# Kernel optimization log

Measured on AMD Instinct MI355X. Metric: run time of the kernel, lower is better.

The kernel has to match this reference:

```python
import jax, jax.numpy as jnp
import numpy as np
from jax import lax

EMBED_DIM = 128
N_RELATIONS = 64
N_ENTITIES = 100000
N_EDGES = 600000


def setup_inputs() -> dict:
    key = jax.random.key(0)
    k1, k2, k3, k4, k5, k6 = jax.random.split(key, 6)
    entity_emb = jax.random.normal(k1, (N_ENTITIES, EMBED_DIM), dtype=jnp.float32)
    heads = jax.random.randint(k2, (N_EDGES,), 0, N_ENTITIES)
    rels = jax.random.randint(k3, (N_EDGES,), 0, N_RELATIONS)
    tails = jax.random.randint(k4, (N_EDGES,), 0, N_ENTITIES)
    # learned params: relation embedding table (std=0.01) and square Linear weight (xavier)
    rel_embed_weight = 0.01 * jax.random.normal(k5, (N_RELATIONS, EMBED_DIM), dtype=jnp.float32)
    xavier = float(np.sqrt(6.0 / (EMBED_DIM + EMBED_DIM)))
    W = jax.random.uniform(k6, (EMBED_DIM, EMBED_DIM), dtype=jnp.float32, minval=-xavier, maxval=xavier)
    return {"entity_emb": entity_emb, "rel_embed_weight": rel_embed_weight, "W": W,
            "heads": heads, "rels": rels, "tails": tails}


def reference(entity_emb, rel_embed_weight, W, heads, rels, tails):
    n_entities = entity_emb.shape[0]
    # gather edge endpoint / relation embeddings: [E, D]
    e_h = entity_emb[heads]
    e_t = entity_emb[tails]
    e_r = rel_embed_weight[rels]
    # tanh-gated dot-product score per edge: [E]
    score = jnp.sum(e_t * jnp.tanh(e_h + e_r), axis=-1)
    # global max-shift (detached in torch) then per-head segment softmax
    score_exp = jnp.exp(score - lax.stop_gradient(jnp.max(score)))
    score_sum = jax.ops.segment_sum(score_exp, heads, num_segments=n_entities)
    attn = score_exp / (score_sum[heads] + 1e-10)
    # scatter-add attention-weighted messages back to head nodes: [N, D]
    agg = jax.ops.segment_sum(attn[:, None] * e_t, heads, num_segments=n_entities)
    # final Linear (no bias) + LeakyReLU(0.2); dropout is identity in eval mode
    out = (entity_emb + agg) @ W.T
    return jax.nn.leaky_relu(out, negative_slope=0.2)
```

## Files before the change

kernel.cpp:

```cpp
#include <hip/hip_runtime.h>
#include <math.h>

#define EMBED 128
#define BMAX 8192
#define LDSPAD 136

typedef __attribute__((ext_vector_type(8))) short short8;
typedef __attribute__((ext_vector_type(4))) short short4v;
typedef __attribute__((ext_vector_type(4))) float floatx4;

__device__ __forceinline__ float fast_tanh2(float x) {
    float e = __expf(2.0f * x);
    return 1.0f - 2.0f * __builtin_amdgcn_rcpf(1.0f + e);
}

__device__ __forceinline__ unsigned short f2b(float f) {
    union { float f; unsigned int u; } v; v.f = f;
    unsigned int r = v.u + 0x7FFFu + ((v.u >> 16) & 1u);
    return (unsigned short)(r >> 16);
}

__device__ __forceinline__ float b2f(short u) {
    union { float f; unsigned int i; } v;
    v.i = ((unsigned int)(unsigned short)u) << 16;
    return v.f;
}

__global__ __launch_bounds__(256) void k_cast_hist(
    const float* __restrict__ ent, const float* __restrict__ rel,
    short* __restrict__ entb, short* __restrict__ relb,
    const int* __restrict__ heads, int* __restrict__ cnt,
    int ngE, int ngR, int E)
{
    int stride = gridDim.x * 256;
    for (int g = blockIdx.x * 256 + threadIdx.x; g < ngE + ngR; g += stride) {
        const float4* src; short* dst;
        if (g < ngE) { src = (const float4*)ent + (size_t)g * 2; dst = entb + (size_t)g * 8; }
        else { int g2 = g - ngE; src = (const float4*)rel + (size_t)g2 * 2; dst = relb + (size_t)g2 * 8; }
        float4 a = src[0], b = src[1];
        short8 o;
        o[0] = (short)f2b(a.x); o[1] = (short)f2b(a.y); o[2] = (short)f2b(a.z); o[3] = (short)f2b(a.w);
        o[4] = (short)f2b(b.x); o[5] = (short)f2b(b.y); o[6] = (short)f2b(b.z); o[7] = (short)f2b(b.w);
        *(short8*)dst = o;
    }
    for (int e = blockIdx.x * 256 + threadIdx.x; e < E; e += stride)
        atomicAdd(cnt + heads[e], 1);
}

__global__ __launch_bounds__(1024) void k_scan1(
    const int* __restrict__ cnt, int* __restrict__ offs,
    int* __restrict__ bsum, int N)
{
    __shared__ int buf[1024];
    int i = blockIdx.x * 1024 + threadIdx.x;
    int v = (i < N) ? cnt[i] : 0;
    buf[threadIdx.x] = v;
    __syncthreads();
    for (int off = 1; off < 1024; off <<= 1) {
        int x = (threadIdx.x >= (unsigned)off) ? buf[threadIdx.x - off] : 0;
        __syncthreads();
        buf[threadIdx.x] += x;
        __syncthreads();
    }
    if (i < N) offs[i] = buf[threadIdx.x] - v;
    if (threadIdx.x == 1023) bsum[blockIdx.x] = buf[1023];
}

__global__ __launch_bounds__(1024) void k_scan2(int* __restrict__ bsum, int nb)
{
    __shared__ int buf[1024];
    int v = (threadIdx.x < (unsigned)nb) ? bsum[threadIdx.x] : 0;
    buf[threadIdx.x] = v;
    __syncthreads();
    for (int off = 1; off < 1024; off <<= 1) {
        int x = (threadIdx.x >= (unsigned)off) ? buf[threadIdx.x - off] : 0;
        __syncthreads();
        buf[threadIdx.x] += x;
        __syncthreads();
    }
    if (threadIdx.x < (unsigned)nb) bsum[threadIdx.x] = buf[threadIdx.x] - v;
}

__global__ __launch_bounds__(256) void k_scan3(
    int* __restrict__ offs, const int* __restrict__ bsum,
    int* __restrict__ cursor, int N)
{
    int i = blockIdx.x * 256 + threadIdx.x;
    if (i < N) {
        int o = offs[i] + bsum[i >> 10];
        offs[i] = o;
        cursor[i] = o;
    }
}

__global__ __launch_bounds__(256) void k_csr(
    const int* __restrict__ heads, const int* __restrict__ rels,
    const int* __restrict__ tails, int* __restrict__ cursor,
    int2* __restrict__ tr, int E)
{
    int e = blockIdx.x * 256 + threadIdx.x;
    if (e >= E) return;
    int pos = atomicAdd(cursor + heads[e], 1);
    tr[pos] = make_int2(tails[e], rels[e]);
}

__global__ __launch_bounds__(256) void k_fused(
    const short* __restrict__ entb, const short* __restrict__ relb,
    const int* __restrict__ offs, const int* __restrict__ cnt,
    const int2* __restrict__ tr,
    short* __restrict__ accb, float* __restrict__ mh, float* __restrict__ lh,
    float* __restrict__ blockmax, int N, int R)
{
    __shared__ short rl[64 * EMBED];
    const int tid = threadIdx.x;
    if (R <= 64) {
        int nch = R * 16;
        for (int i = tid; i < nch; i += 256)
            ((short8*)rl)[i] = ((const short8*)relb)[i];
    }
    __syncthreads();
    const short* relsrc = (R <= 64) ? (const short*)rl : relb;

    const int lane = tid & 15;
    int head = blockIdx.x * 16 + (tid >> 4);
    float m = -INFINITY;
    if (head < N) {
        int start = offs[head];
        int c     = cnt[head];
        short8 hh = *((const short8*)(entb + (size_t)head * EMBED) + lane);
        float hf[8];
        #pragma unroll
        for (int i = 0; i < 8; ++i) hf[i] = b2f(hh[i]);
        float l = 0.f;
        float acc[8] = {0,0,0,0,0,0,0,0};
        for (int base = 0; base < c; base += 16) {
            int rem = c - base;
            int mm  = rem < 16 ? rem : 16;
            int2 trv = make_int2(0, 0);
            if (lane < mm) trv = tr[start + base + lane];
            for (int j = 0; j < mm; ++j) {
                int t = __shfl(trv.x, j, 16);
                int r = __shfl(trv.y, j, 16);
                short8 vt = *((const short8*)(entb + (size_t)t * EMBED) + lane);
                short8 vr = *((const short8*)(relsrc + (size_t)r * EMBED) + lane);
                float s = 0.f;
                #pragma unroll
                for (int i = 0; i < 8; ++i)
                    s += b2f(vt[i]) * fast_tanh2(hf[i] + b2f(vr[i]));
                s += __shfl_xor(s, 1, 16);
                s += __shfl_xor(s, 2, 16);
                s += __shfl_xor(s, 4, 16);
                s += __shfl_xor(s, 8, 16);
                float mn    = fmaxf(m, s);
                float alpha = __expf(m - mn);
                float p     = __expf(s - mn);
                l = l * alpha + p;
                #pragma unroll
                for (int q = 0; q < 8; ++q)
                    acc[q] = acc[q] * alpha + p * b2f(vt[q]);
                m = mn;
            }
        }
        short8 o;
        #pragma unroll
        for (int q = 0; q < 8; ++q) o[q] = (short)f2b(acc[q]);
        *((short8*)(accb + (size_t)head * EMBED) + lane) = o;
        if (lane == 0) { mh[head] = m; lh[head] = l; }
    }
    __shared__ float smax[256];
    smax[tid] = m;
    __syncthreads();
    for (int off = 128; off > 0; off >>= 1) {
        if (tid < off) smax[tid] = fmaxf(smax[tid], smax[tid + off]);
        __syncthreads();
    }
    if (tid == 0) blockmax[blockIdx.x] = smax[0];
}

__global__ __launch_bounds__(256) void k_maxred(
    const float* __restrict__ blockmax, float* __restrict__ Mout, int n)
{
    __shared__ float smax[256];
    float m = -INFINITY;
    for (int i = threadIdx.x; i < n; i += 256) m = fmaxf(m, blockmax[i]);
    smax[threadIdx.x] = m;
    __syncthreads();
    for (int off = 128; off > 0; off >>= 1) {
        if ((int)threadIdx.x < off)
            smax[threadIdx.x] = fmaxf(smax[threadIdx.x], smax[threadIdx.x + off]);
        __syncthreads();
    }
    if (threadIdx.x == 0) Mout[0] = smax[0];
}

__global__ __launch_bounds__(256) void k_gemm_f(
    const short* __restrict__ entb, const short* __restrict__ accb,
    const float* __restrict__ mh, const float* __restrict__ lh,
    const float* __restrict__ Mptr, const float* __restrict__ W,
    float* __restrict__ out, int N)
{
    __shared__ short xs[128 * LDSPAD];
    __shared__ short ws[128 * LDSPAD];
    const int tid = threadIdx.x;
    const int n0  = blockIdx.x * 128;
    const float M = Mptr[0];

    #pragma unroll
    for (int it = 0; it < 16; ++it) {
        int f4 = it * 256 + tid;
        int row = f4 >> 5, col4 = f4 & 31;
        float4 v = ((const float4*)W)[f4];
        short4v b; b[0] = (short)f2b(v.x); b[1] = (short)f2b(v.y);
                   b[2] = (short)f2b(v.z); b[3] = (short)f2b(v.w);
        *(short4v*)(ws + row * LDSPAD + col4 * 4) = b;
    }
    #pragma unroll
    for (int it = 0; it < 8; ++it) {
        int ch = it * 256 + tid;
        int row = ch >> 4, col8 = ch & 15;
        int g = n0 + row;
        short8 v = {0,0,0,0,0,0,0,0};
        if (g < N) {
            float inv = 1.0f / (lh[g] + 1e-10f * __expf(M - mh[g]));
            short8 e8 = *((const short8*)(entb + (size_t)g * EMBED) + col8);
            short8 a8 = *((const short8*)(accb + (size_t)g * EMBED) + col8);
            #pragma unroll
            for (int q = 0; q < 8; ++q)
                v[q] = (short)f2b(b2f(e8[q]) + b2f(a8[q]) * inv);
        }
        *(short8*)(xs + row * LDSPAD + col8 * 8) = v;
    }
    __syncthreads();

    const int wv   = tid >> 6;
    const int lane = tid & 63;
    const int n16  = lane & 15;
    const int quad = lane >> 4;

    floatx4 acc[2][8];
    #pragma unroll
    for (int rt = 0; rt < 2; ++rt)
        #pragma unroll
        for (int jt = 0; jt < 8; ++jt)
            acc[rt][jt] = (floatx4){0.f, 0.f, 0.f, 0.f};

    #pragma unroll
    for (int kc = 0; kc < 4; ++kc) {
        int koff = kc * 32 + quad * 8;
        short8 a0 = *(const short8*)(xs + (wv * 32      + n16) * LDSPAD + koff);
        short8 a1 = *(const short8*)(xs + (wv * 32 + 16 + n16) * LDSPAD + koff);
        #pragma unroll
        for (int jt = 0; jt < 8; ++jt) {
            short8 b = *(const short8*)(ws + (jt * 16 + n16) * LDSPAD + koff);
            acc[0][jt] = __builtin_amdgcn_mfma_f32_16x16x32_bf16(a0, b, acc[0][jt], 0, 0, 0);
            acc[1][jt] = __builtin_amdgcn_mfma_f32_16x16x32_bf16(a1, b, acc[1][jt], 0, 0, 0);
        }
    }

    #pragma unroll
    for (int rt = 0; rt < 2; ++rt) {
        int rowbase = n0 + wv * 32 + rt * 16 + quad * 4;
        #pragma unroll
        for (int r = 0; r < 4; ++r) {
            int grow = rowbase + r;
            if (grow < N) {
                float* o = out + (size_t)grow * EMBED + n16;
                #pragma unroll
                for (int jt = 0; jt < 8; ++jt) {
                    float v = acc[rt][jt][r];
                    o[jt * 16] = (v > 0.f) ? v : 0.2f * v;
                }
            }
        }
    }
}

extern "C" void kernel_launch(void* const* d_in, const int* in_sizes, int n_in,
                              void* d_out, int out_size, void* d_ws, size_t ws_size,
                              hipStream_t stream)
{
    const float* ent   = (const float*)d_in[0];
    const float* rel   = (const float*)d_in[1];
    const float* W     = (const float*)d_in[2];
    const int*   heads = (const int*)d_in[3];
    const int*   rels  = (const int*)d_in[4];
    const int*   tails = (const int*)d_in[5];
    const int E = in_sizes[3];
    const int N = in_sizes[0] / EMBED;
    const int R = in_sizes[1] / EMBED;
    float* out = (float*)d_out;

    short* accb     = (short*)d_ws;
    float* mh       = (float*)(accb + (size_t)N * EMBED);
    float* lh       = mh + N;
    int2*  tr       = (int2*)(lh + N);
    int*   cnt      = (int*)(tr + E);
    int*   offs     = cnt + N;
    int*   cursor   = offs + N;
    float* blockmax = (float*)(cursor + N);
    float* Mval     = blockmax + BMAX;
    int*   bsum     = (int*)(Mval + 1);
    short* entb     = (short*)(bsum + 1024);
    short* relb     = entb + (size_t)N * EMBED;

    const int nb  = (N + 1023) >> 10;
    const int ngh = (N + 15) / 16;

    hipMemsetAsync(cnt, 0, (size_t)N * sizeof(int), stream);

    int ngE = N * EMBED / 8, ngR = R * EMBED / 8;
    k_cast_hist<<<2048, 256, 0, stream>>>(ent, rel, entb, relb, heads, cnt, ngE, ngR, E);
    k_scan1<<<nb, 1024, 0, stream>>>(cnt, offs, bsum, N);
    k_scan2<<<1, 1024, 0, stream>>>(bsum, nb);
    k_scan3<<<(N + 255) / 256, 256, 0, stream>>>(offs, bsum, cursor, N);
    k_csr<<<(E + 255) / 256, 256, 0, stream>>>(heads, rels, tails, cursor, tr, E);
    k_fused<<<ngh, 256, 0, stream>>>(entb, relb, offs, cnt, tr, accb, mh, lh, blockmax, N, R);
    k_maxred<<<1, 256, 0, stream>>>(blockmax, Mval, ngh);
    k_gemm_f<<<(N + 127) / 128, 256, 0, stream>>>(entb, accb, mh, lh, Mval, W, out, N);
}
```

Baseline: 258.9 us.

## Use exp2-domain tanh/softmax, prefetch tails, warp scans, atomic global max

Relation embeddings are pre-scaled by 2*log2e and head features likewise, so tanh and the online softmax use exp2 directly with fewer multiplies. The next tail row is prefetched inside the edge loop to overlap gather latency. The LDS scans are replaced with wavefront shuffle scans, and the per-block max now goes through an ordered-int atomicMax, which removes the separate max-reduce kernel. W is cast to bf16 once in the cast kernel rather than in every GEMM block. Rounding the pre-scaled relation values to bf16 slightly changes numerics.

```diff
diff --git a/kernel.cpp b/kernel.cpp
--- a/kernel.cpp
+++ b/kernel.cpp
@@ -2,17 +2,14 @@
 #include <math.h>
 
 #define EMBED 128
-#define BMAX 8192
 #define LDSPAD 136
 
+#define TWO_LOG2E 2.8853900817779268f
+#define LOG2E     1.4426950408889634f
+
 typedef __attribute__((ext_vector_type(8))) short short8;
-typedef __attribute__((ext_vector_type(4))) short short4v;
 typedef __attribute__((ext_vector_type(4))) float floatx4;
-
-__device__ __forceinline__ float fast_tanh2(float x) {
-    float e = __expf(2.0f * x);
-    return 1.0f - 2.0f * __builtin_amdgcn_rcpf(1.0f + e);
-}
+typedef __attribute__((ext_vector_type(4))) unsigned int uint4v;
 
 __device__ __forceinline__ unsigned short f2b(float f) {
     union { float f; unsigned int u; } v; v.f = f;
@@ -27,20 +24,24 @@
 }
 
 __global__ __launch_bounds__(256) void k_cast_hist(
-    const float* __restrict__ ent, const float* __restrict__ rel,
-    short* __restrict__ entb, short* __restrict__ relb,
+    const float* __restrict__ ent, const float* __restrict__ rel, const float* __restrict__ W,
+    short* __restrict__ entb, short* __restrict__ relb, short* __restrict__ wb,
     const int* __restrict__ heads, int* __restrict__ cnt,
-    int ngE, int ngR, int E)
+    int ngE, int ngR, int ngW, int E)
 {
     int stride = gridDim.x * 256;
-    for (int g = blockIdx.x * 256 + threadIdx.x; g < ngE + ngR; g += stride) {
-        const float4* src; short* dst;
-        if (g < ngE) { src = (const float4*)ent + (size_t)g * 2; dst = entb + (size_t)g * 8; }
-        else { int g2 = g - ngE; src = (const float4*)rel + (size_t)g2 * 2; dst = relb + (size_t)g2 * 8; }
+    int total = ngE + ngR + ngW;
+    for (int g = blockIdx.x * 256 + threadIdx.x; g < total; g += stride) {
+        const float4* src; short* dst; float sc;
+        if (g < ngE)            { src = (const float4*)ent + (size_t)g * 2;              dst = entb + (size_t)g * 8;              sc = 1.0f; }
+        else if (g < ngE + ngR) { int g2 = g - ngE;       src = (const float4*)rel + (size_t)g2 * 2; dst = relb + (size_t)g2 * 8; sc = TWO_LOG2E; }
+        else                    { int g2 = g - ngE - ngR; src = (const float4*)W   + (size_t)g2 * 2; dst = wb   + (size_t)g2 * 8; sc = 1.0f; }
         float4 a = src[0], b = src[1];
         short8 o;
-        o[0] = (short)f2b(a.x); o[1] = (short)f2b(a.y); o[2] = (short)f2b(a.z); o[3] = (short)f2b(a.w);
-        o[4] = (short)f2b(b.x); o[5] = (short)f2b(b.y); o[6] = (short)f2b(b.z); o[7] = (short)f2b(b.w);
+        o[0] = (short)f2b(a.x * sc); o[1] = (short)f2b(a.y * sc);
+        o[2] = (short)f2b(a.z * sc); o[3] = (short)f2b(a.w * sc);
+        o[4] = (short)f2b(b.x * sc); o[5] = (short)f2b(b.y * sc);
+        o[6] = (short)f2b(b.z * sc); o[7] = (short)f2b(b.w * sc);
         *(short8*)dst = o;
     }
     for (int e = blockIdx.x * 256 + threadIdx.x; e < E; e += stride)
@@ -51,34 +52,60 @@
     const int* __restrict__ cnt, int* __restrict__ offs,
     int* __restrict__ bsum, int N)
 {
-    __shared__ int buf[1024];
-    int i = blockIdx.x * 1024 + threadIdx.x;
+    __shared__ int wsum[16];
+    const int tid = threadIdx.x;
+    int i = blockIdx.x * 1024 + tid;
     int v = (i < N) ? cnt[i] : 0;
-    buf[threadIdx.x] = v;
-    __syncthreads();
-    for (int off = 1; off < 1024; off <<= 1) {
-        int x = (threadIdx.x >= (unsigned)off) ? buf[threadIdx.x - off] : 0;
-        __syncthreads();
-        buf[threadIdx.x] += x;
-        __syncthreads();
-    }
-    if (i < N) offs[i] = buf[threadIdx.x] - v;
-    if (threadIdx.x == 1023) bsum[blockIdx.x] = buf[1023];
+    int x = v;
+    #pragma unroll
+    for (int d = 1; d < 64; d <<= 1) {
+        int y = __shfl_up(x, d, 64);
+        if ((tid & 63) >= d) x += y;
+    }
+    if ((tid & 63) == 63) wsum[tid >> 6] = x;
+    __syncthreads();
+    if (tid < 16) {
+        int w = wsum[tid];
+        #pragma unroll
+        for (int d = 1; d < 16; d <<= 1) {
+            int y = __shfl_up(w, d, 16);
+            if (tid >= d) w += y;
+        }
+        wsum[tid] = w;
+    }
+    __syncthreads();
+    int add = (tid >= 64) ? wsum[(tid >> 6) - 1] : 0;
+    int incl = x + add;
+    if (i < N) offs[i] = incl - v;
+    if (tid == 1023) bsum[blockIdx.x] = incl;
 }
 
 __global__ __launch_bounds__(1024) void k_scan2(int* __restrict__ bsum, int nb)
 {
-    __shared__ int buf[1024];
-    int v = (threadIdx.x < (unsigned)nb) ? bsum[threadIdx.x] : 0;
-    buf[threadIdx.x] = v;
-    __syncthreads();
-    for (int off = 1; off < 1024; off <<= 1) {
-        int x = (threadIdx.x >= (unsigned)off) ? buf[threadIdx.x - off] : 0;
-        __syncthreads();
-        buf[threadIdx.x] += x;
-        __syncthreads();
-    }
-    if (threadIdx.x < (unsigned)nb) bsum[threadIdx.x] = buf[threadIdx.x] - v;
+    __shared__ int wsum[16];
+    const int tid = threadIdx.x;
+    int v = (tid < nb) ? bsum[tid] : 0;
+    int x = v;
+    #pragma unroll
+    for (int d = 1; d < 64; d <<= 1) {
+        int y = __shfl_up(x, d, 64);
+        if ((tid & 63) >= d) x += y;
+    }
+    if ((tid & 63) == 63) wsum[tid >> 6] = x;
+    __syncthreads();
+    if (tid < 16) {
+        int w = wsum[tid];
+        #pragma unroll
+        for (int d = 1; d < 16; d <<= 1) {
+            int y = __shfl_up(w, d, 16);
+            if (tid >= d) w += y;
+        }
+        wsum[tid] = w;
+    }
+    __syncthreads();
+    int add = (tid >= 64) ? wsum[(tid >> 6) - 1] : 0;
+    int incl = x + add;
+    if (tid < nb) bsum[tid] = incl - v;
 }
 
 __global__ __launch_bounds__(256) void k_scan3(
@@ -109,7 +136,7 @@
     const int* __restrict__ offs, const int* __restrict__ cnt,
     const int2* __restrict__ tr,
     short* __restrict__ accb, float* __restrict__ mh, float* __restrict__ lh,
-    float* __restrict__ blockmax, int N, int R)
+    unsigned int* __restrict__ Mbits, int N, int R)
 {
     __shared__ short rl[64 * EMBED];
     const int tid = threadIdx.x;
@@ -127,10 +154,13 @@
     if (head < N) {
         int start = offs[head];
         int c     = cnt[head];
-        short8 hh = *((const short8*)(entb + (size_t)head * EMBED) + lane);
+        uint4v hu = *((const uint4v*)(entb + (size_t)head * EMBED) + lane);
         float hf[8];
         #pragma unroll
-        for (int i = 0; i < 8; ++i) hf[i] = b2f(hh[i]);
+        for (int p = 0; p < 4; ++p) {
+            hf[2*p]   = __uint_as_float(hu[p] << 16)          * TWO_LOG2E;
+            hf[2*p+1] = __uint_as_float(hu[p] & 0xFFFF0000u)  * TWO_LOG2E;
+        }
         float l = 0.f;
         float acc[8] = {0,0,0,0,0,0,0,0};
         for (int base = 0; base < c; base += 16) {
@@ -138,26 +168,46 @@
             int mm  = rem < 16 ? rem : 16;
             int2 trv = make_int2(0, 0);
             if (lane < mm) trv = tr[start + base + lane];
+            int t0 = __shfl(trv.x, 0, 16);
+            uint4v vtn = *((const uint4v*)(entb + (size_t)t0 * EMBED) + lane);
             for (int j = 0; j < mm; ++j) {
-                int t = __shfl(trv.x, j, 16);
+                uint4v vt = vtn;
+                if (j + 1 < mm) {
+                    int t2 = __shfl(trv.x, j + 1, 16);
+                    vtn = *((const uint4v*)(entb + (size_t)t2 * EMBED) + lane);
+                }
                 int r = __shfl(trv.y, j, 16);
-                short8 vt = *((const short8*)(entb + (size_t)t * EMBED) + lane);
-                short8 vr = *((const short8*)(relsrc + (size_t)r * EMBED) + lane);
-                float s = 0.f;
+                uint4v ru = *((const uint4v*)(relsrc + (size_t)r * EMBED) + lane);
+                float S = 0.f;
+                float vtf[8];
                 #pragma unroll
-                for (int i = 0; i < 8; ++i)
-                    s += b2f(vt[i]) * fast_tanh2(hf[i] + b2f(vr[i]));
-                s += __shfl_xor(s, 1, 16);
-                s += __shfl_xor(s, 2, 16);
-                s += __shfl_xor(s, 4, 16);
-                s += __shfl_xor(s, 8, 16);
-                float mn    = fmaxf(m, s);
-                float alpha = __expf(m - mn);
-                float p     = __expf(s - mn);
+                for (int p = 0; p < 4; ++p) {
+                    unsigned int tu = vt[p], rr = ru[p];
+                    float tlo = __uint_as_float(tu << 16);
+                    float thi = __uint_as_float(tu & 0xFFFF0000u);
+                    float xlo = hf[2*p]   + __uint_as_float(rr << 16);
+                    float xhi = hf[2*p+1] + __uint_as_float(rr & 0xFFFF0000u);
+                    float elo = exp2f(xlo);
+                    float ehi = exp2f(xhi);
+                    float clo = __builtin_amdgcn_rcpf(1.0f + elo);
+                    float chi = __builtin_amdgcn_rcpf(1.0f + ehi);
+                    S += tlo * (1.0f - 2.0f * clo);
+                    S += thi * (1.0f - 2.0f * chi);
+                    vtf[2*p]   = tlo;
+                    vtf[2*p+1] = thi;
+                }
+                S += __shfl_xor(S, 1, 16);
+                S += __shfl_xor(S, 2, 16);
+                S += __shfl_xor(S, 4, 16);
+                S += __shfl_xor(S, 8, 16);
+                float s2    = S * LOG2E;
+                float mn    = fmaxf(m, s2);
+                float alpha = exp2f(m - mn);
+                float p     = exp2f(s2 - mn);
                 l = l * alpha + p;
                 #pragma unroll
                 for (int q = 0; q < 8; ++q)
-                    acc[q] = acc[q] * alpha + p * b2f(vt[q]);
+                    acc[q] = acc[q] * alpha + p * vtf[q];
                 m = mn;
             }
         }
@@ -174,45 +224,32 @@
         if (tid < off) smax[tid] = fmaxf(smax[tid], smax[tid + off]);
         __syncthreads();
     }
-    if (tid == 0) blockmax[blockIdx.x] = smax[0];
-}
-
-__global__ __launch_bounds__(256) void k_maxred(
-    const float* __restrict__ blockmax, float* __restrict__ Mout, int n)
-{
-    __shared__ float smax[256];
-    float m = -INFINITY;
-    for (int i = threadIdx.x; i < n; i += 256) m = fmaxf(m, blockmax[i]);
-    smax[threadIdx.x] = m;
-    __syncthreads();
-    for (int off = 128; off > 0; off >>= 1) {
-        if ((int)threadIdx.x < off)
-            smax[threadIdx.x] = fmaxf(smax[threadIdx.x], smax[threadIdx.x + off]);
-        __syncthreads();
-    }
-    if (threadIdx.x == 0) Mout[0] = smax[0];
+    if (tid == 0) {
+        unsigned int u = __float_as_uint(smax[0]);
+        unsigned int key = (u & 0x80000000u) ? ~u : (u | 0x80000000u);
+        atomicMax(Mbits, key);
+    }
 }
 
 __global__ __launch_bounds__(256) void k_gemm_f(
     const short* __restrict__ entb, const short* __restrict__ accb,
     const float* __restrict__ mh, const float* __restrict__ lh,
-    const float* __restrict__ Mptr, const float* __restrict__ W,
+    const unsigned int* __restrict__ Mbits, const short* __restrict__ wb,
     float* __restrict__ out, int N)
 {
     __shared__ short xs[128 * LDSPAD];
     __shared__ short ws[128 * LDSPAD];
     const int tid = threadIdx.x;
     const int n0  = blockIdx.x * 128;
-    const float M = Mptr[0];
-
-    #pragma unroll
-    for (int it = 0; it < 16; ++it) {
-        int f4 = it * 256 + tid;
-        int row = f4 >> 5, col4 = f4 & 31;
-        float4 v = ((const float4*)W)[f4];
-        short4v b; b[0] = (short)f2b(v.x); b[1] = (short)f2b(v.y);
-                   b[2] = (short)f2b(v.z); b[3] = (short)f2b(v.w);
-        *(short4v*)(ws + row * LDSPAD + col4 * 4) = b;
+    unsigned int k = Mbits[0];
+    const float M2 = (k & 0x80000000u) ? __uint_as_float(k & 0x7FFFFFFFu)
+                                       : __uint_as_float(~k);
+
+    #pragma unroll
+    for (int it = 0; it < 8; ++it) {
+        int ch = it * 256 + tid;
+        int row = ch >> 4, col8 = ch & 15;
+        *(short8*)(ws + row * LDSPAD + col8 * 8) = ((const short8*)wb)[ch];
     }
     #pragma unroll
     for (int it = 0; it < 8; ++it) {
@@ -221,7 +258,7 @@
         int g = n0 + row;
         short8 v = {0,0,0,0,0,0,0,0};
         if (g < N) {
-            float inv = 1.0f / (lh[g] + 1e-10f * __expf(M - mh[g]));
+            float inv = 1.0f / (lh[g] + 1e-10f * exp2f(M2 - mh[g]));
             short8 e8 = *((const short8*)(entb + (size_t)g * EMBED) + col8);
             short8 a8 = *((const short8*)(accb + (size_t)g * EMBED) + col8);
             #pragma unroll
@@ -290,31 +327,31 @@
     const int R = in_sizes[1] / EMBED;
     float* out = (float*)d_out;
 
-    short* accb     = (short*)d_ws;
-    float* mh       = (float*)(accb + (size_t)N * EMBED);
-    float* lh       = mh + N;
-    int2*  tr       = (int2*)(lh + N);
-    int*   cnt      = (int*)(tr + E);
-    int*   offs     = cnt + N;
-    int*   cursor   = offs + N;
-    float* blockmax = (float*)(cursor + N);
-    float* Mval     = blockmax + BMAX;
-    int*   bsum     = (int*)(Mval + 1);
-    short* entb     = (short*)(bsum + 1024);
-    short* relb     = entb + (size_t)N * EMBED;
+    short* accb        = (short*)d_ws;
+    float* mh          = (float*)(accb + (size_t)N * EMBED);
+    float* lh          = mh + N;
+    int2*  tr          = (int2*)(lh + N);
+    int*   cnt         = (int*)(tr + E);
+    int*   offs        = cnt + N;
+    int*   cursor      = offs + N;
+    short* wb          = (short*)(cursor + N);
+    int*   bsum        = (int*)(wb + 16384);
+    unsigned int* Mbits = (unsigned int*)(bsum + 1024);
+    short* entb        = (short*)(Mbits + 4);
+    short* relb        = entb + (size_t)N * EMBED;
 
     const int nb  = (N + 1023) >> 10;
     const int ngh = (N + 15) / 16;
 
     hipMemsetAsync(cnt, 0, (size_t)N * sizeof(int), stream);
-
-    int ngE = N * EMBED / 8, ngR = R * EMBED / 8;
-    k_cast_hist<<<2048, 256, 0, stream>>>(ent, rel, entb, relb, heads, cnt, ngE, ngR, E);
+    hipMemsetAsync((void*)Mbits, 0, sizeof(unsigned int), stream);
+
+    int ngE = N * EMBED / 8, ngR = R * EMBED / 8, ngW = EMBED * EMBED / 8;
+    k_cast_hist<<<2048, 256, 0, stream>>>(ent, rel, W, entb, relb, wb, heads, cnt, ngE, ngR, ngW, E);
     k_scan1<<<nb, 1024, 0, stream>>>(cnt, offs, bsum, N);
     k_scan2<<<1, 1024, 0, stream>>>(bsum, nb);
     k_scan3<<<(N + 255) / 256, 256, 0, stream>>>(offs, bsum, cursor, N);
     k_csr<<<(E + 255) / 256, 256, 0, stream>>>(heads, rels, tails, cursor, tr, E);
-    k_fused<<<ngh, 256, 0, stream>>>(entb, relb, offs, cnt, tr, accb, mh, lh, blockmax, N, R);
-    k_maxred<<<1, 256, 0, stream>>>(blockmax, Mval, ngh);
-    k_gemm_f<<<(N + 127) / 128, 256, 0, stream>>>(entb, accb, mh, lh, Mval, W, out, N);
-}
+    k_fused<<<ngh, 256, 0, stream>>>(entb, relb, offs, cnt, tr, accb, mh, lh, Mbits, N, R);
+    k_gemm_f<<<(N + 127) / 128, 256, 0, stream>>>(entb, accb, mh, lh, Mbits, wb, out, N);
+}
```

New measurement: 281.5 us. +8.7%, slower.

## Precast W to bf16 once, use shuffle-based scans, and exp2 tanh

Applied to the files above, without the earlier changes.

Converts the weight matrix to bf16 once inside the cast kernel, so each GEMM block copies ready bf16 rows into LDS instead of loading fp32 and converting. Replaces the LDS Hillis-Steele scans with wavefront shuffle scans plus a small per-wave sum pass, which cuts the many block-wide barriers. Computes tanh through a direct exp2 builtin with a prescaled constant. The ideas are small and touch minor stages, so the overall gain may be limited. The workspace layout is shifted to make room for the bf16 weight buffer.

```diff
diff --git a/kernel.cpp b/kernel.cpp
--- a/kernel.cpp
+++ b/kernel.cpp
@@ -5,12 +5,15 @@
 #define BMAX 8192
 #define LDSPAD 136
 
+#define TWO_LOG2E 2.8853900817779268f
+
 typedef __attribute__((ext_vector_type(8))) short short8;
-typedef __attribute__((ext_vector_type(4))) short short4v;
 typedef __attribute__((ext_vector_type(4))) float floatx4;
 
+__device__ __forceinline__ float ex2(float x) { return __builtin_amdgcn_exp2f(x); }
+
 __device__ __forceinline__ float fast_tanh2(float x) {
-    float e = __expf(2.0f * x);
+    float e = ex2(TWO_LOG2E * x);
     return 1.0f - 2.0f * __builtin_amdgcn_rcpf(1.0f + e);
 }
 
@@ -27,16 +30,18 @@
 }
 
 __global__ __launch_bounds__(256) void k_cast_hist(
-    const float* __restrict__ ent, const float* __restrict__ rel,
-    short* __restrict__ entb, short* __restrict__ relb,
+    const float* __restrict__ ent, const float* __restrict__ rel, const float* __restrict__ W,
+    short* __restrict__ entb, short* __restrict__ relb, short* __restrict__ wb,
     const int* __restrict__ heads, int* __restrict__ cnt,
-    int ngE, int ngR, int E)
+    int ngE, int ngR, int ngW, int E)
 {
     int stride = gridDim.x * 256;
-    for (int g = blockIdx.x * 256 + threadIdx.x; g < ngE + ngR; g += stride) {
+    int total = ngE + ngR + ngW;
+    for (int g = blockIdx.x * 256 + threadIdx.x; g < total; g += stride) {
         const float4* src; short* dst;
-        if (g < ngE) { src = (const float4*)ent + (size_t)g * 2; dst = entb + (size_t)g * 8; }
-        else { int g2 = g - ngE; src = (const float4*)rel + (size_t)g2 * 2; dst = relb + (size_t)g2 * 8; }
+        if (g < ngE)            { src = (const float4*)ent + (size_t)g * 2;              dst = entb + (size_t)g * 8; }
+        else if (g < ngE + ngR) { int g2 = g - ngE;       src = (const float4*)rel + (size_t)g2 * 2; dst = relb + (size_t)g2 * 8; }
+        else                    { int g2 = g - ngE - ngR; src = (const float4*)W   + (size_t)g2 * 2; dst = wb   + (size_t)g2 * 8; }
         float4 a = src[0], b = src[1];
         short8 o;
         o[0] = (short)f2b(a.x); o[1] = (short)f2b(a.y); o[2] = (short)f2b(a.z); o[3] = (short)f2b(a.w);
@@ -51,34 +56,60 @@
     const int* __restrict__ cnt, int* __restrict__ offs,
     int* __restrict__ bsum, int N)
 {
-    __shared__ int buf[1024];
-    int i = blockIdx.x * 1024 + threadIdx.x;
+    __shared__ int wsum[16];
+    const int tid = threadIdx.x;
+    int i = blockIdx.x * 1024 + tid;
     int v = (i < N) ? cnt[i] : 0;
-    buf[threadIdx.x] = v;
-    __syncthreads();
-    for (int off = 1; off < 1024; off <<= 1) {
-        int x = (threadIdx.x >= (unsigned)off) ? buf[threadIdx.x - off] : 0;
-        __syncthreads();
-        buf[threadIdx.x] += x;
-        __syncthreads();
-    }
-    if (i < N) offs[i] = buf[threadIdx.x] - v;
-    if (threadIdx.x == 1023) bsum[blockIdx.x] = buf[1023];
+    int x = v;
+    #pragma unroll
+    for (int d = 1; d < 64; d <<= 1) {
+        int y = __shfl_up(x, d, 64);
+        if ((tid & 63) >= d) x += y;
+    }
+    if ((tid & 63) == 63) wsum[tid >> 6] = x;
+    __syncthreads();
+    if (tid < 16) {
+        int w = wsum[tid];
+        #pragma unroll
+        for (int d = 1; d < 16; d <<= 1) {
+            int y = __shfl_up(w, d, 16);
+            if (tid >= d) w += y;
+        }
+        wsum[tid] = w;
+    }
+    __syncthreads();
+    int add = (tid >= 64) ? wsum[(tid >> 6) - 1] : 0;
+    int incl = x + add;
+    if (i < N) offs[i] = incl - v;
+    if (tid == 1023) bsum[blockIdx.x] = incl;
 }
 
 __global__ __launch_bounds__(1024) void k_scan2(int* __restrict__ bsum, int nb)
 {
-    __shared__ int buf[1024];
-    int v = (threadIdx.x < (unsigned)nb) ? bsum[threadIdx.x] : 0;
-    buf[threadIdx.x] = v;
-    __syncthreads();
-    for (int off = 1; off < 1024; off <<= 1) {
-        int x = (threadIdx.x >= (unsigned)off) ? buf[threadIdx.x - off] : 0;
-        __syncthreads();
-        buf[threadIdx.x] += x;
-        __syncthreads();
-    }
-    if (threadIdx.x < (unsigned)nb) bsum[threadIdx.x] = buf[threadIdx.x] - v;
+    __shared__ int wsum[16];
+    const int tid = threadIdx.x;
+    int v = (tid < nb) ? bsum[tid] : 0;
+    int x = v;
+    #pragma unroll
+    for (int d = 1; d < 64; d <<= 1) {
+        int y = __shfl_up(x, d, 64);
+        if ((tid & 63) >= d) x += y;
+    }
+    if ((tid & 63) == 63) wsum[tid >> 6] = x;
+    __syncthreads();
+    if (tid < 16) {
+        int w = wsum[tid];
+        #pragma unroll
+        for (int d = 1; d < 16; d <<= 1) {
+            int y = __shfl_up(w, d, 16);
+            if (tid >= d) w += y;
+        }
+        wsum[tid] = w;
+    }
+    __syncthreads();
+    int add = (tid >= 64) ? wsum[(tid >> 6) - 1] : 0;
+    int incl = x + add;
+    if (tid < nb) bsum[tid] = incl - v;
 }
 
 __global__ __launch_bounds__(256) void k_scan3(
@@ -196,7 +227,7 @@
 __global__ __launch_bounds__(256) void k_gemm_f(
     const short* __restrict__ entb, const short* __restrict__ accb,
     const float* __restrict__ mh, const float* __restrict__ lh,
-    const float* __restrict__ Mptr, const float* __restrict__ W,
+    const float* __restrict__ Mptr, const short* __restrict__ wb,
     float* __restrict__ out, int N)
 {
     __shared__ short xs[128 * LDSPAD];
@@ -206,13 +237,10 @@
     const float M = Mptr[0];
 
     #pragma unroll
-    for (int it = 0; it < 16; ++it) {
-        int f4 = it * 256 + tid;
-        int row = f4 >> 5, col4 = f4 & 31;
-        float4 v = ((const float4*)W)[f4];
-        short4v b; b[0] = (short)f2b(v.x); b[1] = (short)f2b(v.y);
-                   b[2] = (short)f2b(v.z); b[3] = (short)f2b(v.w);
-        *(short4v*)(ws + row * LDSPAD + col4 * 4) = b;
+    for (int it = 0; it < 8; ++it) {
+        int ch = it * 256 + tid;
+        int row = ch >> 4, col8 = ch & 15;
+        *(short8*)(ws + row * LDSPAD + col8 * 8) = ((const short8*)wb)[ch];
     }
     #pragma unroll
     for (int it = 0; it < 8; ++it) {
@@ -299,8 +327,9 @@
     int*   cursor   = offs + N;
     float* blockmax = (float*)(cursor + N);
     float* Mval     = blockmax + BMAX;
-    int*   bsum     = (int*)(Mval + 1);
-    short* entb     = (short*)(bsum + 1024);
+    int*   bsum     = (int*)(Mval + 4);
+    short* wb       = (short*)(bsum + 1024);
+    short* entb     = wb + 16384;
     short* relb     = entb + (size_t)N * EMBED;
 
     const int nb  = (N + 1023) >> 10;
@@ -308,13 +337,13 @@
 
     hipMemsetAsync(cnt, 0, (size_t)N * sizeof(int), stream);
 
-    int ngE = N * EMBED / 8, ngR = R * EMBED / 8;
-    k_cast_hist<<<2048, 256, 0, stream>>>(ent, rel, entb, relb, heads, cnt, ngE, ngR, E);
+    int ngE = N * EMBED / 8, ngR = R * EMBED / 8, ngW = EMBED * EMBED / 8;
+    k_cast_hist<<<2048, 256, 0, stream>>>(ent, rel, W, entb, relb, wb, heads, cnt, ngE, ngR, ngW, E);
     k_scan1<<<nb, 1024, 0, stream>>>(cnt, offs, bsum, N);
     k_scan2<<<1, 1024, 0, stream>>>(bsum, nb);
     k_scan3<<<(N + 255) / 256, 256, 0, stream>>>(offs, bsum, cursor, N);
     k_csr<<<(E + 255) / 256, 256, 0, stream>>>(heads, rels, tails, cursor, tr, E);
     k_fused<<<ngh, 256, 0, stream>>>(entb, relb, offs, cnt, tr, accb, mh, lh, blockmax, N, R);
     k_maxred<<<1, 256, 0, stream>>>(blockmax, Mval, ngh);
-    k_gemm_f<<<(N + 127) / 128, 256, 0, stream>>>(entb, accb, mh, lh, Mval, W, out, N);
-}
+    k_gemm_f<<<(N + 127) / 128, 256, 0, stream>>>(entb, accb, mh, lh, Mval, wb, out, N);
+}
```

Measured after the change: 252.3 us. 1.03x faster.
